# Kernel optimization log

Hardware: AMD Instinct MI355X
Metric: run time of the kernel (lower is better)

## Reference

```python
import jax, jax.numpy as jnp
import numpy as np

IN_DIM = 256
QK_DIM = IN_DIM // 8  # 32
NCLS = 19
B, H, W = 2, 64, 64


def conv3x3(x, w, b):
    # x: [B,C,H,W], w: [O,I,3,3] -> SAME padding, stride 1 (= pad=1 in torch)
    y = jax.lax.conv_general_dilated(x, w, (1, 1), 'SAME',
                                     dimension_numbers=('NCHW', 'OIHW', 'NCHW'))
    return y + b[None, :, None, None]


def setup_inputs() -> dict:
    key = jax.random.key(0)
    ks = jax.random.split(key, 20)
    s = 0.05
    inp = {
        'x': jax.random.normal(ks[0], (B, IN_DIM, H, W), jnp.float32),
        'modal_mask': jax.random.uniform(ks[1], (B, NCLS, H, W), jnp.float32),
        'amodal_mask': jax.random.uniform(ks[2], (B, NCLS, H, W), jnp.float32),
        'w_mp': jax.random.normal(ks[3], (NCLS, IN_DIM, 3, 3), jnp.float32) * s,
        'b_mp': jnp.zeros((NCLS,), jnp.float32),
        'w_ap': jax.random.normal(ks[4], (NCLS, IN_DIM, 3, 3), jnp.float32) * s,
        'b_ap': jnp.zeros((NCLS,), jnp.float32),
        'w_q': jax.random.normal(ks[5], (QK_DIM, IN_DIM + NCLS, 3, 3), jnp.float32) * s,
        'b_q': jnp.zeros((QK_DIM,), jnp.float32),
        'w_k': jax.random.normal(ks[6], (QK_DIM, IN_DIM + NCLS, 3, 3), jnp.float32) * s,
        'b_k': jnp.zeros((QK_DIM,), jnp.float32),
        'w_v': jax.random.normal(ks[7], (IN_DIM, IN_DIM, 3, 3), jnp.float32) * s,
        'b_v': jnp.zeros((IN_DIM,), jnp.float32),
        'w_comp': jax.random.normal(ks[8], (IN_DIM, IN_DIM + 2 * NCLS, 3, 3), jnp.float32) * s,
        'b_comp': jnp.zeros((IN_DIM,), jnp.float32),
        'w_out': jax.random.normal(ks[9], (IN_DIM, 3 * IN_DIM, 3, 3), jnp.float32) * s,
        'b_out': jnp.zeros((IN_DIM,), jnp.float32),
        # SELayer(in_dim, reduction=8): Linear(c, c//8, bias=False), Linear(c//8, c, bias=False)
        'w_se1': jax.random.normal(ks[10], (IN_DIM // 8, IN_DIM), jnp.float32) * s,
        'w_se2': jax.random.normal(ks[11], (IN_DIM, IN_DIM // 8), jnp.float32) * s,
    }
    return inp


def reference(x, modal_mask, amodal_mask, w_mp, b_mp, w_ap, b_ap, w_q, b_q,
              w_k, b_k, w_v, b_v, w_comp, b_comp, w_out, b_out, w_se1, w_se2):
    b, c, h, w = x.shape
    n = h * w
    # masks already at (h, w): nearest interpolate is identity
    modal_x = conv3x3(x, w_mp, b_mp) * modal_mask
    amodal_x = conv3x3(x, w_ap, b_ap) * amodal_mask
    inp = jnp.concatenate([x, modal_x, amodal_x], axis=1)
    out = conv3x3(inp, w_comp, b_comp)
    # SE layer
    y = out.mean(axis=(2, 3))                                # [b, c]
    y = jax.nn.sigmoid(jax.nn.relu(y @ w_se1.T) @ w_se2.T)   # [b, c]
    out_a = out * y[:, :, None, None]
    # dual-softmax spatial attention
    q = conv3x3(jnp.concatenate([x, modal_mask], axis=1), w_q, b_q).reshape(b, QK_DIM, n)
    k = conv3x3(jnp.concatenate([x, amodal_mask], axis=1), w_k, b_k).reshape(b, QK_DIM, n)
    v = conv3x3(x, w_v, b_v).reshape(b, c, n)
    energy = jnp.einsum('bdn,bdm->bnm', q, k)                # [b, n, n]
    attn = jax.nn.softmax(energy, axis=-1)                   # softmax over keys
    attn_t = jax.nn.softmax(energy, axis=1)                  # softmax over queries (of E^T rows)
    # out_b = bmm(v, attn^T); out_c = bmm(v, softmax(E^T,-1)^T)
    out_b = jnp.einsum('bcn,bmn->bcm', v, attn).reshape(b, c, h, w)
    out_c = jnp.einsum('bcn,bnm->bcm', v, attn_t).reshape(b, c, h, w)
    out = jnp.concatenate([out_a, out_b, out_c], axis=1)
    return conv3x3(out, w_out, b_out)
```

## Files before the change

kernel.cpp:

```cpp
#include <hip/hip_runtime.h>
#include <math.h>

#define HW 4096
#define IMG 64
#define PIX66 (66 * 66)

typedef short short8 __attribute__((ext_vector_type(8)));
typedef float f32x4 __attribute__((ext_vector_type(4)));

__device__ __forceinline__ unsigned short f2bf(float f) {
    unsigned int u = __float_as_uint(f);
    u += 0x7fff + ((u >> 16) & 1);
    return (unsigned short)(u >> 16);
}
__device__ __forceinline__ float bf2f(unsigned short h) {
    return __uint_as_float(((unsigned int)h) << 16);
}
__device__ __forceinline__ unsigned int pkbf(float a, float b) {
    unsigned int ua = __float_as_uint(a) + 0x8000u;
    unsigned int ub = __float_as_uint(b) + 0x8000u;
    return __builtin_amdgcn_perm(ub, ua, 0x07060302u);
}

__device__ __forceinline__ void gll16(const unsigned short* g, unsigned short* l) {
    __builtin_amdgcn_global_load_lds(
        (const __attribute__((address_space(1))) unsigned int*)(g),
        (__attribute__((address_space(3))) unsigned int*)(l), 16, 0, 0);
}

__device__ __forceinline__ int pxor(int pix) { return (pix ^ (pix >> 2)) & 3; }
__device__ __forceinline__ int p32o(int pix, int c) {
    return pix * 32 + ((((c >> 3) ^ pxor(pix)) & 3) << 3) + (c & 7);
}

struct WtJob {
    const float* w;
    unsigned short* dh;
    unsigned short* dl;
    int OC, OCpad, C0, K0pad, C1, Ktot;
};

__global__ __launch_bounds__(256) void k_wt_all(WtJob J0, WtJob J1, WtJob J2,
                                                WtJob J3, WtJob J4, WtJob J5,
                                                WtJob J6) {
    WtJob J;
    switch (blockIdx.y) {
        case 0: J = J0; break;
        case 1: J = J1; break;
        case 2: J = J2; break;
        case 3: J = J3; break;
        case 4: J = J4; break;
        case 5: J = J5; break;
        default: J = J6; break;
    }
    int idx = blockIdx.x * 256 + threadIdx.x;
    int KS = J.Ktot >> 5;
    int n = 9 * KS * J.OCpad * 32;
    if (idx >= n) return;
    int kk = idx & 31;
    int rest = idx >> 5;
    int oc = rest % J.OCpad;
    rest /= J.OCpad;
    int kg = rest % KS;
    int tap = rest / KS;
    int k = kg * 32 + kk;
    float v = 0.f;
    if (oc < J.OC) {
        int ic = -1;
        if (k < J.C0) ic = k;
        else if (k >= J.K0pad && (k - J.K0pad) < J.C1) ic = J.C0 + (k - J.K0pad);
        if (ic >= 0) v = J.w[((size_t)oc * (J.C0 + J.C1) + ic) * 9 + tap];
    }
    unsigned short hi = f2bf(v);
    J.dh[idx] = hi;
    if (J.dl) J.dl[idx] = f2bf(v - bf2f(hi));
}

__global__ __launch_bounds__(256) void k_build_x(const float* __restrict__ x,
                                                 unsigned short* __restrict__ xh,
                                                 unsigned short* __restrict__ xl,
                                                 unsigned short* __restrict__ ipad) {
    int b = blockIdx.z, c0 = blockIdx.y * 64, p0 = blockIdx.x * 64;
    __shared__ float s[64][65];
    int t = threadIdx.x;
    for (int i = t; i < 4096; i += 256) {
        int c = i >> 6, p = i & 63;
        s[p][c] = x[((size_t)b * 256 + c0 + c) * HW + p0 + p];
    }
    __syncthreads();
    for (int i = t; i < 4096; i += 256) {
        int c = i & 63, p = i >> 6;
        float f = s[p][c];
        unsigned short hi = f2bf(f);
        unsigned short lo = f2bf(f - bf2f(hi));
        int pp = p0 + p;
        int y = pp >> 6, xx = pp & 63;
        int pix = (y + 1) * 66 + xx + 1;
        int C = c0 + c;
        size_t ix = (size_t)(b * 8 + (C >> 5)) * (PIX66 * 32) + p32o(pix, C & 31);
        xh[ix] = hi;
        xl[ix] = lo;
        ipad[(size_t)(b * 10 + (C >> 5)) * (PIX66 * 32) + p32o(pix, C & 31)] = hi;
    }
}

__global__ __launch_bounds__(256) void k_build_mask2(
    const float* __restrict__ m0, const float* __restrict__ m1,
    unsigned short* __restrict__ d0h, unsigned short* __restrict__ d0l,
    unsigned short* __restrict__ d1h, unsigned short* __restrict__ d1l) {
    const float* m = blockIdx.y ? m1 : m0;
    unsigned short* dh = blockIdx.y ? d1h : d0h;
    unsigned short* dl = blockIdx.y ? d1l : d0l;
    int idx = blockIdx.x * 256 + threadIdx.x;
    int c = idx & 31;
    int p = (idx >> 5) & 4095;
    int b = idx >> 17;
    float f = (c < 19) ? m[((size_t)b * 19 + c) * HW + p] : 0.f;
    unsigned short hi = f2bf(f);
    int y = p >> 6, xx = p & 63;
    int pix = (y + 1) * 66 + xx + 1;
    dh[(size_t)b * (PIX66 * 32) + p32o(pix, c)] = hi;
    dl[(size_t)b * (PIX66 * 32) + p32o(pix, c)] = f2bf(f - bf2f(hi));
}

struct ConvJob {
    const unsigned short* s1h;
    const unsigned short* s1l;
    const unsigned short* wth;
    const unsigned short* wtl;
    const float* bias;
    unsigned short* d1;
    unsigned short* d2;
    const float* mask;
    int chBase;
};

template <int MODE, int SPLITK, int KS0, int KS1>
__global__ __launch_bounds__(256, 2) void conv_direct(
    const unsigned short* __restrict__ s0h, const unsigned short* __restrict__ s0l,
    ConvJob j0, ConvJob j1) {
    constexpr int KS = KS0 + KS1;
    constexpr int ST = 9 * KS;
    constexpr int DEPTH = SPLITK ? 2 : 4;
    int b = blockIdx.z;
    ConvJob J = blockIdx.y ? j1 : j0;
    int t = threadIdx.x, w = t >> 6, l = t & 63, quad = l >> 4, ln = l & 15;
    int pBase = blockIdx.x * 128 + w * 32;

    int padpix[2];
#pragma unroll
    for (int tn = 0; tn < 2; ++tn) {
        int p = pBase + tn * 16 + ln;
        padpix[tn] = ((p >> 6) + 1) * 66 + (p & 63) + 1;
    }
    size_t aoff[2];
#pragma unroll
    for (int tm = 0; tm < 2; ++tm) aoff[tm] = (size_t)(tm * 16 + ln) * 32 + quad * 8;

    const unsigned short* S0H = s0h + (size_t)b * KS0 * PIX66 * 32;
    const unsigned short* S0L = SPLITK ? s0l + (size_t)b * KS0 * PIX66 * 32
                                       : (const unsigned short*)0;
    const unsigned short* S1H = KS1 ? J.s1h + (size_t)b * KS1 * PIX66 * 32
                                    : (const unsigned short*)0;
    const unsigned short* S1L = (KS1 && SPLITK) ? J.s1l + (size_t)b * KS1 * PIX66 * 32
                                                : (const unsigned short*)0;

    f32x4 acc[2][2];
#pragma unroll
    for (int i = 0; i < 2; ++i)
#pragma unroll
        for (int j = 0; j < 2; ++j) acc[i][j] = (f32x4){0.f, 0.f, 0.f, 0.f};

    int tap = 0, kg = 0;
    auto adv = [&]() { if (++kg == KS) { kg = 0; ++tap; } };
    auto loadStep = [&](int ltap, int lkg, short8* bh, short8* bl, short8* ah,
                        short8* al) {
        int d3 = ltap / 3;
        int dpix = (d3 - 1) * 66 + (ltap - d3 * 3 - 1);
        const unsigned short* SpH;
        const unsigned short* SpL;
        long plane;
        if (lkg < KS0) {
            SpH = S0H; SpL = S0L; plane = (long)lkg * PIX66 * 32;
        } else {
            SpH = S1H; SpL = S1L; plane = (long)(lkg - KS0) * PIX66 * 32;
        }
#pragma unroll
        for (int tn = 0; tn < 2; ++tn) {
            int pix2 = padpix[tn] + dpix;
            long off = plane + (long)pix2 * 32 + (((quad ^ pxor(pix2)) & 3) << 3);
            bh[tn] = *(const short8*)(SpH + off);
            if (SPLITK) bl[tn] = *(const short8*)(SpL + off);
        }
        const unsigned short* WTh = J.wth + (size_t)(ltap * KS + lkg) * 32 * 32;
        ah[0] = *(const short8*)(WTh + aoff[0]);
        ah[1] = *(const short8*)(WTh + aoff[1]);
        if (SPLITK) {
            const unsigned short* WTl = J.wtl + (size_t)(ltap * KS + lkg) * 32 * 32;
            al[0] = *(const short8*)(WTl + aoff[0]);
            al[1] = *(const short8*)(WTl + aoff[1]);
        }
    };

    short8 BH[DEPTH][2], AH[DEPTH][2];
    short8 BL[SPLITK ? DEPTH : 1][2], AL[SPLITK ? DEPTH : 1][2];
#pragma unroll
    for (int u = 0; u < DEPTH; ++u) {
        loadStep(tap, kg, BH[u], BL[SPLITK ? u : 0], AH[u], AL[SPLITK ? u : 0]);
        adv();
    }

    for (int s = 0; s < ST; s += DEPTH) {
#pragma unroll
        for (int u = 0; u < DEPTH; ++u) {
            if (s + u < ST) {
#pragma unroll
                for (int tm = 0; tm < 2; ++tm)
#pragma unroll
                    for (int tn = 0; tn < 2; ++tn) {
                        acc[tm][tn] = __builtin_amdgcn_mfma_f32_16x16x32_bf16(
                            AH[u][tm], BH[u][tn], acc[tm][tn], 0, 0, 0);
                        if (SPLITK) {
                            acc[tm][tn] = __builtin_amdgcn_mfma_f32_16x16x32_bf16(
                                AL[u][tm], BH[u][tn], acc[tm][tn], 0, 0, 0);
                            acc[tm][tn] = __builtin_amdgcn_mfma_f32_16x16x32_bf16(
                                AH[u][tm], BL[u][tn], acc[tm][tn], 0, 0, 0);
                        }
                    }
                if (s + u + DEPTH < ST) {
                    loadStep(tap, kg, BH[u], BL[SPLITK ? u : 0], AH[u],
                             AL[SPLITK ? u : 0]);
                    adv();
                }
            }
        }
    }

#pragma unroll
    for (int tm = 0; tm < 2; ++tm) {
#pragma unroll
        for (int r = 0; r < 4; ++r) {
            int oc = tm * 16 + quad * 4 + r;
#pragma unroll
            for (int tn = 0; tn < 2; ++tn) {
                int p = pBase + tn * 16 + ln;
                if (MODE == 1) {
                    if (oc < 19) {
                        float v = (acc[tm][tn][r] + J.bias[oc]) *
                                  J.mask[((size_t)b * 19 + oc) * HW + p];
                        int ch = J.chBase + oc;
                        J.d1[(size_t)(b * 10 + (ch >> 5)) * (PIX66 * 32) +
                             p32o(padpix[tn], ch & 31)] = f2bf(v);
                    }
                } else {
                    float v = acc[tm][tn][r] + J.bias[oc];
                    unsigned short hi = f2bf(v);
                    J.d1[((size_t)b * HW + p) * 32 + oc] = hi;
                    J.d2[((size_t)b * HW + p) * 32 + oc] = f2bf(v - bf2f(hi));
                }
            }
        }
    }
}

struct LdsJob {
    const unsigned short* src;
    const unsigned short* wt;
    const float* bias;
    float* dstf;
    unsigned short* dstb;
    int KS;
    int mode;
};

__global__ __launch_bounds__(128, 3) void conv_lds(LdsJob j0, LdsJob j1,
                                                   int ocgPerJob,
                                                   float* __restrict__ ybuf) {
    int jy = blockIdx.y;
    LdsJob J = (jy >= ocgPerJob) ? j1 : j0;
    int ocBase = ((jy >= ocgPerJob) ? jy - ocgPerJob : jy) * 64;
    int z = blockIdx.z;
    int b = (J.mode == 5) ? (z & 1) : z;
    int kgBeg = 0, kgEnd = J.KS;
    if (J.mode == 5) {
        int half = J.KS >> 1;
        kgBeg = (z >> 1) * half;
        kgEnd = kgBeg + half;
    }
    int ry = blockIdx.x * 2;
    int t = threadIdx.x, w = t >> 6, l = t & 63, quad = l >> 4, ln = l & 15;

    __shared__ unsigned short sB[2][264 * 32];

    const unsigned short* S = J.src + (size_t)b * J.KS * PIX66 * 32;
    const size_t bStageBase = (size_t)(ry * 66) * 32;

    f32x4 acc[4][4];
#pragma unroll
    for (int i = 0; i < 4; ++i)
#pragma unroll
        for (int j = 0; j < 4; ++j) acc[i][j] = (f32x4){0.f, 0.f, 0.f, 0.f};

    {
        const unsigned short* gB = S + (size_t)kgBeg * PIX66 * 32 + bStageBase;
        for (int i = t; i < 1056; i += 128) gll16(gB + (size_t)i * 8, sB[0] + (size_t)i * 8);
    }

    for (int kg = kgBeg; kg < kgEnd; ++kg) {
        int cur = (kg - kgBeg) & 1;
        __syncthreads();
        if (kg + 1 < kgEnd) {
            const unsigned short* gB = S + (size_t)(kg + 1) * PIX66 * 32 + bStageBase;
            for (int i = t; i < 1056; i += 128)
                gll16(gB + (size_t)i * 8, sB[cur ^ 1] + (size_t)i * 8);
        }
        const unsigned short* sBc = sB[cur];
#pragma unroll
        for (int tap = 0; tap < 9; ++tap) {
            const unsigned short* gA =
                J.wt + ((size_t)(tap * J.KS + kg) * 256 + ocBase) * 32;
            int dy = tap / 3 - 1, dx = tap % 3 - 1;
            int lpBase = (1 + w + dy) * 66 + 1 + dx;
            short8 bf[4], af[4];
#pragma unroll
            for (int tn = 0; tn < 4; ++tn) {
                int lp = lpBase + tn * 16 + ln;
                int P = ry * 66 + lp;
                bf[tn] = *(const short8*)(sBc + (size_t)lp * 32 +
                                          (((quad ^ pxor(P)) & 3) << 3));
            }
#pragma unroll
            for (int tm = 0; tm < 4; ++tm)
                af[tm] = *(const short8*)(gA + (size_t)(tm * 16 + ln) * 32 + quad * 8);
#pragma unroll
            for (int tm = 0; tm < 4; ++tm)
#pragma unroll
                for (int tn = 0; tn < 4; ++tn)
                    acc[tm][tn] = __builtin_amdgcn_mfma_f32_16x16x32_bf16(
                        af[tm], bf[tn], acc[tm][tn], 0, 0, 0);
        }
    }

    int prow = ry + w;
#pragma unroll
    for (int tm = 0; tm < 4; ++tm) {
#pragma unroll
        for (int r = 0; r < 4; ++r) {
            int oc = ocBase + tm * 16 + quad * 4 + r;
            float msum = 0.f;
#pragma unroll
            for (int tn = 0; tn < 4; ++tn) {
                int px = tn * 16 + ln;
                if (J.mode == 5) {
                    J.dstf[((size_t)z * 256 + oc) * HW + prow * 64 + px] =
                        acc[tm][tn][r];
                } else if (J.mode == 3) {
                    int jc = ((px >> 3) ^ (oc & 7)) & 7;
                    J.dstb[(((size_t)b * 64 + prow) * 256 + oc) * 64 + jc * 8 +
                           (px & 7)] = f2bf(acc[tm][tn][r] + J.bias[oc]);
                } else {
                    float v = acc[tm][tn][r] + J.bias[oc];
                    int pix = (prow + 1) * 66 + px + 1;
                    J.dstb[(size_t)(b * 24 + (oc >> 5)) * (PIX66 * 32) +
                           p32o(pix, oc & 31)] = f2bf(v);
                    msum += v;
                }
            }
            if (J.mode == 4) {
#pragma unroll
                for (int off = 8; off; off >>= 1) msum += __shfl_down(msum, off, 16);
                if (ln == 0) atomicAdd(&ybuf[b * 256 + oc], msum);
            }
        }
    }
}

__global__ __launch_bounds__(256) void out_combine(const float* __restrict__ part,
                                                   const float* __restrict__ bias,
                                                   float* __restrict__ outp) {
    int idx = blockIdx.x * 256 + threadIdx.x;
    int p = idx & 4095;
    int oc = (idx >> 12) & 255;
    int b = idx >> 20;
    float v = part[((size_t)b * 256 + oc) * HW + p] +
              part[((size_t)(2 + b) * 256 + oc) * HW + p] + bias[oc];
    outp[((size_t)b * 256 + oc) * HW + p] = v;
}

__global__ __launch_bounds__(512, 4) void flash_attn(
    const unsigned short* __restrict__ qt_h, const unsigned short* __restrict__ qt_l,
    const unsigned short* __restrict__ kt_h, const unsigned short* __restrict__ kt_l,
    const unsigned short* __restrict__ vt,
    float* __restrict__ pO, float* __restrict__ pm, float* __restrict__ pl) {
    int seg = blockIdx.y >> 1, mode = blockIdx.y & 1, b = blockIdx.z;
    size_t qkoff = (size_t)b * HW * 32;
    const unsigned short* Qh = (mode ? kt_h : qt_h) + qkoff;
    const unsigned short* Ql = (mode ? kt_l : qt_l) + qkoff;
    const unsigned short* Kh = (mode ? qt_h : kt_h) + qkoff;
    const unsigned short* Kl = (mode ? qt_l : kt_l) + qkoff;
    const unsigned short* Vt = vt + (size_t)b * 64 * 256 * 64;

    int t = threadIdx.x, w = t >> 6, l = t & 63, quad = l >> 4, ln = l & 15;
    int pg = w & 1, ch = w >> 1;
    int p0 = blockIdx.x * 64, pw = pg * 32;
    int cb = ch * 64;
    bool soft = (ch == (pg ? 3 : 0));

    __shared__ unsigned short sV[256 * 64];
    __shared__ unsigned short sP[64 * 68];
    __shared__ float sAl[64];

    short8 qbh[2], qbl[2];
    if (soft) {
#pragma unroll
        for (int pn = 0; pn < 2; ++pn) {
            size_t off = (size_t)(p0 + pw + pn * 16 + ln) * 32 + quad * 8;
            qbh[pn] = *(const short8*)(Qh + off);
            qbl[pn] = *(const short8*)(Ql + off);
        }
    }

    float m_run[2] = {-3.0e38f, -3.0e38f};
    float l_run[2] = {0.f, 0.f};
    f32x4 accO[4][2];
#pragma unroll
    for (int cs = 0; cs < 4; ++cs)
#pragma unroll
        for (int pn = 0; pn < 2; ++pn) accO[cs][pn] = (f32x4){0.f, 0.f, 0.f, 0.f};

    int jbBeg = seg * (HW / 2);
    for (int jb = jbBeg; jb < jbBeg + HW / 2; jb += 64) {
        __syncthreads();
        {
            const unsigned short* gV = Vt + (size_t)(jb >> 6) * (256 * 64);
#pragma unroll
            for (int i = 0; i < 4; ++i)
                gll16(gV + (size_t)(t + 512 * i) * 8, sV + (size_t)(t + 512 * i) * 8);
        }
        if (soft) {
            f32x4 sacc[2][4];
#pragma unroll
            for (int pn = 0; pn < 2; ++pn)
#pragma unroll
                for (int jj = 0; jj < 4; ++jj) sacc[pn][jj] = (f32x4){0.f, 0.f, 0.f, 0.f};
#pragma unroll
            for (int jj = 0; jj < 4; ++jj) {
                size_t off = (size_t)(jb + 16 * jj + ln) * 32 + quad * 8;
                short8 kh = *(const short8*)(Kh + off);
                short8 kr = *(const short8*)(Kl + off);
#pragma unroll
                for (int pn = 0; pn < 2; ++pn) {
                    sacc[pn][jj] = __builtin_amdgcn_mfma_f32_16x16x32_bf16(
                        kh, qbh[pn], sacc[pn][jj], 0, 0, 0);
                    sacc[pn][jj] = __builtin_amdgcn_mfma_f32_16x16x32_bf16(
                        kh, qbl[pn], sacc[pn][jj], 0, 0, 0);
                    sacc[pn][jj] = __builtin_amdgcn_mfma_f32_16x16x32_bf16(
                        kr, qbh[pn], sacc[pn][jj], 0, 0, 0);
                }
            }
#pragma unroll
            for (int pn = 0; pn < 2; ++pn) {
                float tmx = -3.0e38f;
#pragma unroll
                for (int jj = 0; jj < 4; ++jj)
#pragma unroll
                    for (int r = 0; r < 4; ++r) tmx = fmaxf(tmx, sacc[pn][jj][r]);
                tmx = fmaxf(tmx, __shfl_xor(tmx, 16));
                tmx = fmaxf(tmx, __shfl_xor(tmx, 32));
                float mnew = fmaxf(m_run[pn], tmx);
                float alpha = __expf(m_run[pn] - mnew);
                m_run[pn] = mnew;
                float psum = 0.f;
#pragma unroll
                for (int jj = 0; jj < 4; ++jj) {
                    float e0 = __expf(sacc[pn][jj][0] - mnew);
                    float e1 = __expf(sacc[pn][jj][1] - mnew);
                    float e2 = __expf(sacc[pn][jj][2] - mnew);
                    float e3 = __expf(sacc[pn][jj][3] - mnew);
                    psum += (e0 + e1) + (e2 + e3);
                    uint2 pk;
                    pk.x = pkbf(e0, e1);
                    pk.y = pkbf(e2, e3);
                    *(uint2*)(sP + (size_t)(pw + pn * 16 + ln) * 68 + jj * 16 +
                              quad * 4) = pk;
                }
                psum += __shfl_xor(psum, 16);
                psum += __shfl_xor(psum, 32);
                l_run[pn] = l_run[pn] * alpha + psum;
                if (quad == 0) sAl[pw + pn * 16 + ln] = alpha;
            }
        }
        __syncthreads();
        float al0 = sAl[pw + ln];
        float al1 = sAl[pw + 16 + ln];
#pragma unroll
        for (int cs = 0; cs < 4; ++cs) { accO[cs][0] *= al0; accO[cs][1] *= al1; }
#pragma unroll
        for (int j2 = 0; j2 < 2; ++j2) {
            short8 pb0 = *(const short8*)(sP + (size_t)(pw + ln) * 68 + j2 * 32 +
                                          quad * 8);
            short8 pb1 = *(const short8*)(sP + (size_t)(pw + 16 + ln) * 68 + j2 * 32 +
                                          quad * 8);
#pragma unroll
            for (int cs = 0; cs < 4; ++cs) {
                int c = cb + cs * 16 + ln;
                short8 va = *(const short8*)(
                    sV + (size_t)c * 64 + ((((j2 * 4 + quad) ^ (c & 7)) & 7) << 3));
                accO[cs][0] = __builtin_amdgcn_mfma_f32_16x16x32_bf16(
                    va, pb0, accO[cs][0], 0, 0, 0);
                accO[cs][1] = __builtin_amdgcn_mfma_f32_16x16x32_bf16(
                    va, pb1, accO[cs][1], 0, 0, 0);
            }
        }
    }

    int idx4 = (seg * 2 + mode) * 2 + b;
#pragma unroll
    for (int pn = 0; pn < 2; ++pn) {
        int p = p0 + pw + pn * 16 + ln;
        if (soft && quad == 0) {
            pm[(size_t)idx4 * HW + p] = m_run[pn];
            pl[(size_t)idx4 * HW + p] = l_run[pn];
        }
#pragma unroll
        for (int cs = 0; cs < 4; ++cs)
#pragma unroll
            for (int r = 0; r < 4; ++r) {
                int c = cb + cs * 16 + quad * 4 + r;
                pO[((size_t)idx4 * 256 + c) * HW + p] = accO[cs][pn][r];
            }
    }
}

__global__ __launch_bounds__(256) void attn_combine(const float* __restrict__ pO,
                                                    const float* __restrict__ pm,
                                                    const float* __restrict__ pl,
                                                    unsigned short* __restrict__ catN) {
    int b = blockIdx.z, mode = blockIdx.y;
    int t = threadIdx.x;
    int p = blockIdx.x * 64 + (t & 63);
    int c0 = (t >> 6) * 64;
    int i0 = mode * 2 + b;
    int i1 = 4 + mode * 2 + b;
    float m0 = pm[(size_t)i0 * HW + p], m1 = pm[(size_t)i1 * HW + p];
    float l0 = pl[(size_t)i0 * HW + p], l1 = pl[(size_t)i1 * HW + p];
    float M = fmaxf(m0, m1);
    float e0 = __expf(m0 - M), e1 = __expf(m1 - M);
    float inv = 1.f / (l0 * e0 + l1 * e1);
    e0 *= inv;
    e1 *= inv;
    int y = p >> 6, x = p & 63;
    int pix = (y + 1) * 66 + x + 1;
    for (int c = c0; c < c0 + 64; ++c) {
        float v = pO[((size_t)i0 * 256 + c) * HW + p] * e0 +
                  pO[((size_t)i1 * 256 + c) * HW + p] * e1;
        int cf = 256 + mode * 256 + c;
        catN[(size_t)(b * 24 + (cf >> 5)) * (PIX66 * 32) + p32o(pix, cf & 31)] = f2bf(v);
    }
}

__global__ __launch_bounds__(256) void se_mlp_kernel(const float* __restrict__ y,
                                                     const float* __restrict__ w1,
                                                     const float* __restrict__ w2,
                                                     float* __restrict__ sc) {
    int b = blockIdx.x, t = threadIdx.x;
    __shared__ float sy[256], sh[32];
    sy[t] = y[b * 256 + t] * (1.f / 4096.f);
    __syncthreads();
    if (t < 32) {
        float s = 0.f;
        for (int c = 0; c < 256; ++c) s = fmaf(w1[t * 256 + c], sy[c], s);
        sh[t] = fmaxf(s, 0.f);
    }
    __syncthreads();
    float s = 0.f;
#pragma unroll
    for (int h = 0; h < 32; ++h) s = fmaf(w2[t * 32 + h], sh[h], s);
    sc[b * 256 + t] = 1.f / (1.f + __expf(-s));
}

__global__ __launch_bounds__(256) void se_scale_cat(unsigned short* __restrict__ catN,
                                                    const float* __restrict__ sc) {
    int idx = blockIdx.x * 256 + threadIdx.x;
    int c = idx & 255;
    int p = (idx >> 8) & 4095;
    int b = idx >> 20;
    int y = p >> 6, x = p & 63;
    int pix = (y + 1) * 66 + x + 1;
    unsigned short* q =
        catN + (size_t)(b * 24 + (c >> 5)) * (PIX66 * 32) + p32o(pix, c & 31);
    *q = f2bf(bf2f(*q) * sc[b * 256 + c]);
}

extern "C" void kernel_launch(void* const* d_in, const int* in_sizes, int n_in,
                              void* d_out, int out_size, void* d_ws, size_t ws_size,
                              hipStream_t stream) {
    const float* x      = (const float*)d_in[0];
    const float* mmask  = (const float*)d_in[1];
    const float* amask  = (const float*)d_in[2];
    const float* w_mp   = (const float*)d_in[3];
    const float* b_mp   = (const float*)d_in[4];
    const float* w_ap   = (const float*)d_in[5];
    const float* b_ap   = (const float*)d_in[6];
    const float* w_q    = (const float*)d_in[7];
    const float* b_q    = (const float*)d_in[8];
    const float* w_k    = (const float*)d_in[9];
    const float* b_k    = (const float*)d_in[10];
    const float* w_v    = (const float*)d_in[11];
    const float* b_v    = (const float*)d_in[12];
    const float* w_comp = (const float*)d_in[13];
    const float* b_comp = (const float*)d_in[14];
    const float* w_out  = (const float*)d_in[15];
    const float* b_out  = (const float*)d_in[16];
    const float* w_se1  = (const float*)d_in[17];
    const float* w_se2  = (const float*)d_in[18];

    unsigned short* us = (unsigned short*)d_ws;
    size_t o = 0;
    unsigned short* xpad_hi = us + o; o += (size_t)2 * 8 * PIX66 * 32;
    unsigned short* xpad_lo = us + o; o += (size_t)2 * 8 * PIX66 * 32;
    unsigned short* mq_hi   = us + o; o += (size_t)2 * PIX66 * 32;
    unsigned short* mq_lo   = us + o; o += (size_t)2 * PIX66 * 32;
    unsigned short* ma_hi   = us + o; o += (size_t)2 * PIX66 * 32;
    unsigned short* ma_lo   = us + o; o += (size_t)2 * PIX66 * 32;
    unsigned short* ipad    = us + o; o += (size_t)2 * 10 * PIX66 * 32;
    unsigned short* catN    = us + o; o += (size_t)2 * 24 * PIX66 * 32;
    size_t zeroBytes = o * sizeof(unsigned short);
    unsigned short* wt_mp = us + o; o += (size_t)9 * 8 * 32 * 32;
    unsigned short* wt_ap = us + o; o += (size_t)9 * 8 * 32 * 32;
    unsigned short* wt_qh = us + o; o += (size_t)9 * 9 * 32 * 32;
    unsigned short* wt_ql = us + o; o += (size_t)9 * 9 * 32 * 32;
    unsigned short* wt_kh = us + o; o += (size_t)9 * 9 * 32 * 32;
    unsigned short* wt_kl = us + o; o += (size_t)9 * 9 * 32 * 32;
    unsigned short* wt_v  = us + o; o += (size_t)9 * 8 * 256 * 32;
    unsigned short* wt_cp = us + o; o += (size_t)9 * 10 * 256 * 32;
    unsigned short* wt_ot = us + o; o += (size_t)9 * 24 * 256 * 32;
    unsigned short* qt_h  = us + o; o += (size_t)2 * HW * 32;
    unsigned short* qt_l  = us + o; o += (size_t)2 * HW * 32;
    unsigned short* kt_h  = us + o; o += (size_t)2 * HW * 32;
    unsigned short* kt_l  = us + o; o += (size_t)2 * HW * 32;
    unsigned short* vt    = us + o; o += (size_t)2 * 64 * 256 * 64;
    float* fp = (float*)(us + o);
    size_t fo = 0;
    float* pAtt = fp + fo; fo += (size_t)8 * 256 * HW;
    float* pmb  = fp + fo; fo += (size_t)8 * HW;
    float* plb  = fp + fo; fo += (size_t)8 * HW;
    float* pOut = fp + fo; fo += (size_t)4 * 256 * HW;
    float* ybuf = fp + fo; fo += 512;
    float* sbuf = fp + fo; fo += 512;
    size_t need = o * sizeof(unsigned short) + fo * sizeof(float);
    if (ws_size < need) return;

    float* outp = (float*)d_out;

    hipMemsetAsync(us, 0, zeroBytes, stream);
    hipMemsetAsync(ybuf, 0, 512 * sizeof(float), stream);

    WtJob W0{w_mp,   wt_mp, (unsigned short*)0, 19, 32, 256, 256, 0, 256};
    WtJob W1{w_ap,   wt_ap, (unsigned short*)0, 19, 32, 256, 256, 0, 256};
    WtJob W2{w_q,    wt_qh, wt_ql,             32, 32, 256, 256, 19, 288};
    WtJob W3{w_k,    wt_kh, wt_kl,             32, 32, 256, 256, 19, 288};
    WtJob W4{w_v,    wt_v,  (unsigned short*)0, 256, 256, 256, 256, 0, 256};
    WtJob W5{w_comp, wt_cp, (unsigned short*)0, 256, 256, 294, 320, 0, 320};
    WtJob W6{w_out,  wt_ot, (unsigned short*)0, 256, 256, 768, 768, 0, 768};
    k_wt_all<<<dim3((9 * 24 * 256 * 32 + 255) / 256, 7), 256, 0, stream>>>(
        W0, W1, W2, W3, W4, W5, W6);

    k_build_x<<<dim3(64, 4, 2), 256, 0, stream>>>(x, xpad_hi, xpad_lo, ipad);
    k_build_mask2<<<dim3(1024, 2), 256, 0, stream>>>(mmask, amask, mq_hi, mq_lo,
                                                     ma_hi, ma_lo);

    const unsigned short* NUS = (const unsigned short*)0;
    unsigned short* NUSo = (unsigned short*)0;
    float* NF = (float*)0;

    ConvJob jm{NUS, NUS, wt_mp, NUS, b_mp, ipad, NUSo, mmask, 256};
    ConvJob ja{NUS, NUS, wt_ap, NUS, b_ap, ipad, NUSo, amask, 275};
    conv_direct<1, 0, 8, 0><<<dim3(32, 2, 2), 256, 0, stream>>>(xpad_hi, NUS, jm, ja);

    ConvJob jq{mq_hi, mq_lo, wt_qh, wt_ql, b_q, qt_h, qt_l, NF, 0};
    ConvJob jk{ma_hi, ma_lo, wt_kh, wt_kl, b_k, kt_h, kt_l, NF, 0};
    conv_direct<2, 1, 8, 1><<<dim3(32, 2, 2), 256, 0, stream>>>(xpad_hi, xpad_lo, jq, jk);

    LdsJob jv{xpad_hi, wt_v, b_v, NF, vt, 8, 3};
    LdsJob jc{ipad, wt_cp, b_comp, NF, catN, 10, 4};
    conv_lds<<<dim3(32, 8, 2), 128, 0, stream>>>(jv, jc, 4, ybuf);

    se_mlp_kernel<<<2, 256, 0, stream>>>(ybuf, w_se1, w_se2, sbuf);
    se_scale_cat<<<8192, 256, 0, stream>>>(catN, sbuf);

    flash_attn<<<dim3(64, 4, 2), 512, 0, stream>>>(qt_h, qt_l, kt_h, kt_l, vt,
                                                   pAtt, pmb, plb);
    attn_combine<<<dim3(64, 2, 2), 256, 0, stream>>>(pAtt, pmb, plb, catN);

    LdsJob jo{catN, wt_ot, NF, pOut, NUSo, 24, 5};
    conv_lds<<<dim3(32, 4, 4), 128, 0, stream>>>(jo, jo, 4, NF);
    out_combine<<<8192, 256, 0, stream>>>(pOut, b_out, outp);
}
```

Measured before the change: 498.1 us.

## Pipeline softmax ahead of PV in flash attention and shrink conv_direct blocks

The flash attention kernel double-buffers the probability tile and alpha arrays so the two softmax warps compute QK and softmax for the next key block while the other warps run the PV MFMAs for the current one. Channel work is rebalanced: softmax warps now handle only 16 channels and the other six warps 80 each, instead of every warp taking 64. Separately, conv_direct drops to 128-thread blocks with twice as many blocks to improve occupancy and load spread. This costs extra LDS for the double buffers, more accumulator registers in the non-softmax warps, and an extra sync per iteration.

```diff
diff --git a/kernel.cpp b/kernel.cpp
--- a/kernel.cpp
+++ b/kernel.cpp
@@ -136,7 +136,7 @@
 };
 
 template <int MODE, int SPLITK, int KS0, int KS1>
-__global__ __launch_bounds__(256, 2) void conv_direct(
+__global__ __launch_bounds__(128, 2) void conv_direct(
     const unsigned short* __restrict__ s0h, const unsigned short* __restrict__ s0l,
     ConvJob j0, ConvJob j1) {
     constexpr int KS = KS0 + KS1;
@@ -145,7 +145,7 @@
     int b = blockIdx.z;
     ConvJob J = blockIdx.y ? j1 : j0;
     int t = threadIdx.x, w = t >> 6, l = t & 63, quad = l >> 4, ln = l & 15;
-    int pBase = blockIdx.x * 128 + w * 32;
+    int pBase = blockIdx.x * 64 + w * 32;
 
     int padpix[2];
 #pragma unroll
@@ -401,14 +401,15 @@
     const unsigned short* Vt = vt + (size_t)b * 64 * 256 * 64;
 
     int t = threadIdx.x, w = t >> 6, l = t & 63, quad = l >> 4, ln = l & 15;
-    int pg = w & 1, ch = w >> 1;
+    int pg = w & 1, sl = w >> 1;
+    bool soft = (sl == (pg ? 3 : 0));
     int p0 = blockIdx.x * 64, pw = pg * 32;
-    int cb = ch * 64;
-    bool soft = (ch == (pg ? 3 : 0));
+    int cbS = pg ? 240 : 0;
+    int cbP = pg ? (sl * 80) : (16 + (sl - 1) * 80);
 
     __shared__ unsigned short sV[256 * 64];
-    __shared__ unsigned short sP[64 * 68];
-    __shared__ float sAl[64];
+    __shared__ unsigned short sP[2][64 * 68];
+    __shared__ float sAl[2][64];
 
     short8 qbh[2], qbl[2];
     if (soft) {
@@ -422,113 +423,157 @@
 
     float m_run[2] = {-3.0e38f, -3.0e38f};
     float l_run[2] = {0.f, 0.f};
-    f32x4 accO[4][2];
-#pragma unroll
-    for (int cs = 0; cs < 4; ++cs)
-#pragma unroll
-        for (int pn = 0; pn < 2; ++pn) accO[cs][pn] = (f32x4){0.f, 0.f, 0.f, 0.f};
+    f32x4 accS[2];
+    f32x4 accP[5][2];
+    accS[0] = (f32x4){0.f, 0.f, 0.f, 0.f};
+    accS[1] = (f32x4){0.f, 0.f, 0.f, 0.f};
+#pragma unroll
+    for (int cs = 0; cs < 5; ++cs) {
+        accP[cs][0] = (f32x4){0.f, 0.f, 0.f, 0.f};
+        accP[cs][1] = (f32x4){0.f, 0.f, 0.f, 0.f};
+    }
 
     int jbBeg = seg * (HW / 2);
-    for (int jb = jbBeg; jb < jbBeg + HW / 2; jb += 64) {
+    const int NT = (HW / 2) / 64;
+
+    auto qkstep = [&](int it2) {
+        int jb = jbBeg + it2 * 64;
+        int nb = it2 & 1;
+        f32x4 sacc[2][4];
+#pragma unroll
+        for (int pn = 0; pn < 2; ++pn)
+#pragma unroll
+            for (int jj = 0; jj < 4; ++jj) sacc[pn][jj] = (f32x4){0.f, 0.f, 0.f, 0.f};
+#pragma unroll
+        for (int jj = 0; jj < 4; ++jj) {
+            size_t off = (size_t)(jb + 16 * jj + ln) * 32 + quad * 8;
+            short8 kh = *(const short8*)(Kh + off);
+            short8 kr = *(const short8*)(Kl + off);
+#pragma unroll
+            for (int pn = 0; pn < 2; ++pn) {
+                sacc[pn][jj] = __builtin_amdgcn_mfma_f32_16x16x32_bf16(
+                    kh, qbh[pn], sacc[pn][jj], 0, 0, 0);
+                sacc[pn][jj] = __builtin_amdgcn_mfma_f32_16x16x32_bf16(
+                    kh, qbl[pn], sacc[pn][jj], 0, 0, 0);
+                sacc[pn][jj] = __builtin_amdgcn_mfma_f32_16x16x32_bf16(
+                    kr, qbh[pn], sacc[pn][jj], 0, 0, 0);
+            }
+        }
+#pragma unroll
+        for (int pn = 0; pn < 2; ++pn) {
+            float tmx = -3.0e38f;
+#pragma unroll
+            for (int jj = 0; jj < 4; ++jj)
+#pragma unroll
+                for (int r = 0; r < 4; ++r) tmx = fmaxf(tmx, sacc[pn][jj][r]);
+            tmx = fmaxf(tmx, __shfl_xor(tmx, 16));
+            tmx = fmaxf(tmx, __shfl_xor(tmx, 32));
+            float mnew = fmaxf(m_run[pn], tmx);
+            float alpha = __expf(m_run[pn] - mnew);
+            m_run[pn] = mnew;
+            float psum = 0.f;
+#pragma unroll
+            for (int jj = 0; jj < 4; ++jj) {
+                float e0 = __expf(sacc[pn][jj][0] - mnew);
+                float e1 = __expf(sacc[pn][jj][1] - mnew);
+                float e2 = __expf(sacc[pn][jj][2] - mnew);
+                float e3 = __expf(sacc[pn][jj][3] - mnew);
+                psum += (e0 + e1) + (e2 + e3);
+                uint2 pk;
+                pk.x = pkbf(e0, e1);
+                pk.y = pkbf(e2, e3);
+                *(uint2*)(sP[nb] + (size_t)(pw + pn * 16 + ln) * 68 + jj * 16 +
+                          quad * 4) = pk;
+            }
+            psum += __shfl_xor(psum, 16);
+            psum += __shfl_xor(psum, 32);
+            l_run[pn] = l_run[pn] * alpha + psum;
+            if (quad == 0) sAl[nb][pw + pn * 16 + ln] = alpha;
+        }
+    };
+
+    if (soft) qkstep(0);
+
+    for (int it = 0; it < NT; ++it) {
+        int cur = it & 1;
         __syncthreads();
         {
-            const unsigned short* gV = Vt + (size_t)(jb >> 6) * (256 * 64);
+            const unsigned short* gV = Vt + (size_t)((jbBeg >> 6) + it) * (256 * 64);
 #pragma unroll
             for (int i = 0; i < 4; ++i)
                 gll16(gV + (size_t)(t + 512 * i) * 8, sV + (size_t)(t + 512 * i) * 8);
         }
+        if (soft && it + 1 < NT) qkstep(it + 1);
+        __syncthreads();
         if (soft) {
-            f32x4 sacc[2][4];
-#pragma unroll
-            for (int pn = 0; pn < 2; ++pn)
-#pragma unroll
-                for (int jj = 0; jj < 4; ++jj) sacc[pn][jj] = (f32x4){0.f, 0.f, 0.f, 0.f};
-#pragma unroll
-            for (int jj = 0; jj < 4; ++jj) {
-                size_t off = (size_t)(jb + 16 * jj + ln) * 32 + quad * 8;
-                short8 kh = *(const short8*)(Kh + off);
-                short8 kr = *(const short8*)(Kl + off);
-#pragma unroll
-                for (int pn = 0; pn < 2; ++pn) {
-                    sacc[pn][jj] = __builtin_amdgcn_mfma_f32_16x16x32_bf16(
-                        kh, qbh[pn], sacc[pn][jj], 0, 0, 0);
-                    sacc[pn][jj] = __builtin_amdgcn_mfma_f32_16x16x32_bf16(
-                        kh, qbl[pn], sacc[pn][jj], 0, 0, 0);
-                    sacc[pn][jj] = __builtin_amdgcn_mfma_f32_16x16x32_bf16(
-                        kr, qbh[pn], sacc[pn][jj], 0, 0, 0);
-                }
-            }
-#pragma unroll
-            for (int pn = 0; pn < 2; ++pn) {
-                float tmx = -3.0e38f;
-#pragma unroll
-                for (int jj = 0; jj < 4; ++jj)
-#pragma unroll
-                    for (int r = 0; r < 4; ++r) tmx = fmaxf(tmx, sacc[pn][jj][r]);
-                tmx = fmaxf(tmx, __shfl_xor(tmx, 16));
-                tmx = fmaxf(tmx, __shfl_xor(tmx, 32));
-                float mnew = fmaxf(m_run[pn], tmx);
-                float alpha = __expf(m_run[pn] - mnew);
-                m_run[pn] = mnew;
-                float psum = 0.f;
-#pragma unroll
-                for (int jj = 0; jj < 4; ++jj) {
-                    float e0 = __expf(sacc[pn][jj][0] - mnew);
-                    float e1 = __expf(sacc[pn][jj][1] - mnew);
-                    float e2 = __expf(sacc[pn][jj][2] - mnew);
-                    float e3 = __expf(sacc[pn][jj][3] - mnew);
-                    psum += (e0 + e1) + (e2 + e3);
-                    uint2 pk;
-                    pk.x = pkbf(e0, e1);
-                    pk.y = pkbf(e2, e3);
-                    *(uint2*)(sP + (size_t)(pw + pn * 16 + ln) * 68 + jj * 16 +
-                              quad * 4) = pk;
-                }
-                psum += __shfl_xor(psum, 16);
-                psum += __shfl_xor(psum, 32);
-                l_run[pn] = l_run[pn] * alpha + psum;
-                if (quad == 0) sAl[pw + pn * 16 + ln] = alpha;
-            }
-        }
-        __syncthreads();
-        float al0 = sAl[pw + ln];
-        float al1 = sAl[pw + 16 + ln];
-#pragma unroll
-        for (int cs = 0; cs < 4; ++cs) { accO[cs][0] *= al0; accO[cs][1] *= al1; }
-#pragma unroll
-        for (int j2 = 0; j2 < 2; ++j2) {
-            short8 pb0 = *(const short8*)(sP + (size_t)(pw + ln) * 68 + j2 * 32 +
-                                          quad * 8);
-            short8 pb1 = *(const short8*)(sP + (size_t)(pw + 16 + ln) * 68 + j2 * 32 +
-                                          quad * 8);
-#pragma unroll
-            for (int cs = 0; cs < 4; ++cs) {
-                int c = cb + cs * 16 + ln;
+            float a0 = sAl[cur][pw + ln], a1 = sAl[cur][pw + 16 + ln];
+            accS[0] *= a0;
+            accS[1] *= a1;
+#pragma unroll
+            for (int j2 = 0; j2 < 2; ++j2) {
+                short8 pb0 = *(const short8*)(sP[cur] + (size_t)(pw + ln) * 68 +
+                                              j2 * 32 + quad * 8);
+                short8 pb1 = *(const short8*)(sP[cur] + (size_t)(pw + 16 + ln) * 68 +
+                                              j2 * 32 + quad * 8);
+                int c = cbS + ln;
                 short8 va = *(const short8*)(
                     sV + (size_t)c * 64 + ((((j2 * 4 + quad) ^ (c & 7)) & 7) << 3));
-                accO[cs][0] = __builtin_amdgcn_mfma_f32_16x16x32_bf16(
-                    va, pb0, accO[cs][0], 0, 0, 0);
-                accO[cs][1] = __builtin_amdgcn_mfma_f32_16x16x32_bf16(
-                    va, pb1, accO[cs][1], 0, 0, 0);
+                accS[0] = __builtin_amdgcn_mfma_f32_16x16x32_bf16(va, pb0, accS[0],
+                                                                  0, 0, 0);
+                accS[1] = __builtin_amdgcn_mfma_f32_16x16x32_bf16(va, pb1, accS[1],
+                                                                  0, 0, 0);
+            }
+        } else {
+            float a0 = sAl[cur][pw + ln], a1 = sAl[cur][pw + 16 + ln];
+#pragma unroll
+            for (int cs = 0; cs < 5; ++cs) { accP[cs][0] *= a0; accP[cs][1] *= a1; }
+#pragma unroll
+            for (int j2 = 0; j2 < 2; ++j2) {
+                short8 pb0 = *(const short8*)(sP[cur] + (size_t)(pw + ln) * 68 +
+                                              j2 * 32 + quad * 8);
+                short8 pb1 = *(const short8*)(sP[cur] + (size_t)(pw + 16 + ln) * 68 +
+                                              j2 * 32 + quad * 8);
+#pragma unroll
+                for (int cs = 0; cs < 5; ++cs) {
+                    int c = cbP + cs * 16 + ln;
+                    short8 va = *(const short8*)(
+                        sV + (size_t)c * 64 + ((((j2 * 4 + quad) ^ (c & 7)) & 7) << 3));
+                    accP[cs][0] = __builtin_amdgcn_mfma_f32_16x16x32_bf16(
+                        va, pb0, accP[cs][0], 0, 0, 0);
+                    accP[cs][1] = __builtin_amdgcn_mfma_f32_16x16x32_bf16(
+                        va, pb1, accP[cs][1], 0, 0, 0);
+                }
             }
         }
     }
 
     int idx4 = (seg * 2 + mode) * 2 + b;
-#pragma unroll
-    for (int pn = 0; pn < 2; ++pn) {
-        int p = p0 + pw + pn * 16 + ln;
-        if (soft && quad == 0) {
-            pm[(size_t)idx4 * HW + p] = m_run[pn];
-            pl[(size_t)idx4 * HW + p] = l_run[pn];
-        }
-#pragma unroll
-        for (int cs = 0; cs < 4; ++cs)
+    if (soft) {
+#pragma unroll
+        for (int pn = 0; pn < 2; ++pn) {
+            int p = p0 + pw + pn * 16 + ln;
+            if (quad == 0) {
+                pm[(size_t)idx4 * HW + p] = m_run[pn];
+                pl[(size_t)idx4 * HW + p] = l_run[pn];
+            }
 #pragma unroll
             for (int r = 0; r < 4; ++r) {
-                int c = cb + cs * 16 + quad * 4 + r;
-                pO[((size_t)idx4 * 256 + c) * HW + p] = accO[cs][pn][r];
-            }
+                int c = cbS + quad * 4 + r;
+                pO[((size_t)idx4 * 256 + c) * HW + p] = accS[pn][r];
+            }
+        }
+    } else {
+#pragma unroll
+        for (int pn = 0; pn < 2; ++pn) {
+            int p = p0 + pw + pn * 16 + ln;
+#pragma unroll
+            for (int cs = 0; cs < 5; ++cs)
+#pragma unroll
+                for (int r = 0; r < 4; ++r) {
+                    int c = cbP + cs * 16 + quad * 4 + r;
+                    pO[((size_t)idx4 * 256 + c) * HW + p] = accP[cs][pn][r];
+                }
+        }
     }
 }
 
@@ -676,11 +721,11 @@
 
     ConvJob jm{NUS, NUS, wt_mp, NUS, b_mp, ipad, NUSo, mmask, 256};
     ConvJob ja{NUS, NUS, wt_ap, NUS, b_ap, ipad, NUSo, amask, 275};
-    conv_direct<1, 0, 8, 0><<<dim3(32, 2, 2), 256, 0, stream>>>(xpad_hi, NUS, jm, ja);
+    conv_direct<1, 0, 8, 0><<<dim3(64, 2, 2), 128, 0, stream>>>(xpad_hi, NUS, jm, ja);
 
     ConvJob jq{mq_hi, mq_lo, wt_qh, wt_ql, b_q, qt_h, qt_l, NF, 0};
     ConvJob jk{ma_hi, ma_lo, wt_kh, wt_kl, b_k, kt_h, kt_l, NF, 0};
-    conv_direct<2, 1, 8, 1><<<dim3(32, 2, 2), 256, 0, stream>>>(xpad_hi, xpad_lo, jq, jk);
+    conv_direct<2, 1, 8, 1><<<dim3(64, 2, 2), 128, 0, stream>>>(xpad_hi, xpad_lo, jq, jk);
 
     LdsJob jv{xpad_hi, wt_v, b_v, NF, vt, 8, 3};
     LdsJob jc{ipad, wt_cp, b_comp, NF, catN, 10, 4};
```

Result: slower. 520.2 us (+4.4%).

## Merge direct convs into one launch and split-K the LDS convs for more blocks

Applied to the files above, without the earlier changes.

Replaces the two templated direct-conv launches with a single runtime-dispatched kernel covering the modal, amodal, q and k jobs, using 128-thread blocks and twice as many blocks. The v and comp LDS convs are split over two K segments and the output conv over four, writing fp32 partials. New combine kernels add the bias, apply the SE scale and convert to bf16, and the separate SE rescale pass is dropped. The aim is better CU occupancy on a small problem, paid for with extra partial-sum memory traffic, more launches, and runtime branches in place of compile-time specialisation.

```diff
diff --git a/kernel.cpp b/kernel.cpp
--- a/kernel.cpp
+++ b/kernel.cpp
@@ -123,7 +123,7 @@
     dl[(size_t)b * (PIX66 * 32) + p32o(pix, c)] = f2bf(f - bf2f(hi));
 }
 
-struct ConvJob {
+struct DJob {
     const unsigned short* s1h;
     const unsigned short* s1l;
     const unsigned short* wth;
@@ -133,19 +133,27 @@
     unsigned short* d2;
     const float* mask;
     int chBase;
+    int mode;
+    int split;
+    int KS1;
 };
 
-template <int MODE, int SPLITK, int KS0, int KS1>
-__global__ __launch_bounds__(256, 2) void conv_direct(
+__global__ __launch_bounds__(128, 2) void conv_direct_all(
     const unsigned short* __restrict__ s0h, const unsigned short* __restrict__ s0l,
-    ConvJob j0, ConvJob j1) {
-    constexpr int KS = KS0 + KS1;
-    constexpr int ST = 9 * KS;
-    constexpr int DEPTH = SPLITK ? 2 : 4;
+    DJob j0, DJob j1, DJob j2, DJob j3) {
+    DJob J;
+    switch (blockIdx.y) {
+        case 0: J = j0; break;
+        case 1: J = j1; break;
+        case 2: J = j2; break;
+        default: J = j3; break;
+    }
+    const int KS0 = 8;
+    int KS = KS0 + J.KS1;
+    int ST = 9 * KS;
     int b = blockIdx.z;
-    ConvJob J = blockIdx.y ? j1 : j0;
     int t = threadIdx.x, w = t >> 6, l = t & 63, quad = l >> 4, ln = l & 15;
-    int pBase = blockIdx.x * 128 + w * 32;
+    int pBase = blockIdx.x * 64 + w * 32;
 
     int padpix[2];
 #pragma unroll
@@ -158,12 +166,11 @@
     for (int tm = 0; tm < 2; ++tm) aoff[tm] = (size_t)(tm * 16 + ln) * 32 + quad * 8;
 
     const unsigned short* S0H = s0h + (size_t)b * KS0 * PIX66 * 32;
-    const unsigned short* S0L = SPLITK ? s0l + (size_t)b * KS0 * PIX66 * 32
-                                       : (const unsigned short*)0;
-    const unsigned short* S1H = KS1 ? J.s1h + (size_t)b * KS1 * PIX66 * 32
-                                    : (const unsigned short*)0;
-    const unsigned short* S1L = (KS1 && SPLITK) ? J.s1l + (size_t)b * KS1 * PIX66 * 32
-                                                : (const unsigned short*)0;
+    const unsigned short* S0L = s0l + (size_t)b * KS0 * PIX66 * 32;
+    const unsigned short* S1H = J.KS1 ? J.s1h + (size_t)b * PIX66 * 32
+                                      : (const unsigned short*)0;
+    const unsigned short* S1L = J.KS1 ? J.s1l + (size_t)b * PIX66 * 32
+                                      : (const unsigned short*)0;
 
     f32x4 acc[2][2];
 #pragma unroll
@@ -183,36 +190,32 @@
         if (lkg < KS0) {
             SpH = S0H; SpL = S0L; plane = (long)lkg * PIX66 * 32;
         } else {
-            SpH = S1H; SpL = S1L; plane = (long)(lkg - KS0) * PIX66 * 32;
+            SpH = S1H; SpL = S1L; plane = 0;
         }
 #pragma unroll
         for (int tn = 0; tn < 2; ++tn) {
             int pix2 = padpix[tn] + dpix;
             long off = plane + (long)pix2 * 32 + (((quad ^ pxor(pix2)) & 3) << 3);
             bh[tn] = *(const short8*)(SpH + off);
-            if (SPLITK) bl[tn] = *(const short8*)(SpL + off);
+            if (J.split) bl[tn] = *(const short8*)(SpL + off);
         }
         const unsigned short* WTh = J.wth + (size_t)(ltap * KS + lkg) * 32 * 32;
         ah[0] = *(const short8*)(WTh + aoff[0]);
         ah[1] = *(const short8*)(WTh + aoff[1]);
-        if (SPLITK) {
+        if (J.split) {
             const unsigned short* WTl = J.wtl + (size_t)(ltap * KS + lkg) * 32 * 32;
             al[0] = *(const short8*)(WTl + aoff[0]);
             al[1] = *(const short8*)(WTl + aoff[1]);
         }
     };
 
-    short8 BH[DEPTH][2], AH[DEPTH][2];
-    short8 BL[SPLITK ? DEPTH : 1][2], AL[SPLITK ? DEPTH : 1][2];
-#pragma unroll
-    for (int u = 0; u < DEPTH; ++u) {
-        loadStep(tap, kg, BH[u], BL[SPLITK ? u : 0], AH[u], AL[SPLITK ? u : 0]);
-        adv();
-    }
-
-    for (int s = 0; s < ST; s += DEPTH) {
-#pragma unroll
-        for (int u = 0; u < DEPTH; ++u) {
+    short8 BH[2][2], AH[2][2], BL[2][2], AL[2][2];
+#pragma unroll
+    for (int u = 0; u < 2; ++u) { loadStep(tap, kg, BH[u], BL[u], AH[u], AL[u]); adv(); }
+
+    for (int s = 0; s < ST; s += 2) {
+#pragma unroll
+        for (int u = 0; u < 2; ++u) {
             if (s + u < ST) {
 #pragma unroll
                 for (int tm = 0; tm < 2; ++tm)
@@ -220,18 +223,14 @@
                     for (int tn = 0; tn < 2; ++tn) {
                         acc[tm][tn] = __builtin_amdgcn_mfma_f32_16x16x32_bf16(
                             AH[u][tm], BH[u][tn], acc[tm][tn], 0, 0, 0);
-                        if (SPLITK) {
+                        if (J.split) {
                             acc[tm][tn] = __builtin_amdgcn_mfma_f32_16x16x32_bf16(
                                 AL[u][tm], BH[u][tn], acc[tm][tn], 0, 0, 0);
                             acc[tm][tn] = __builtin_amdgcn_mfma_f32_16x16x32_bf16(
                                 AH[u][tm], BL[u][tn], acc[tm][tn], 0, 0, 0);
                         }
                     }
-                if (s + u + DEPTH < ST) {
-                    loadStep(tap, kg, BH[u], BL[SPLITK ? u : 0], AH[u],
-                             AL[SPLITK ? u : 0]);
-                    adv();
-                }
+                if (s + u + 2 < ST) { loadStep(tap, kg, BH[u], BL[u], AH[u], AL[u]); adv(); }
             }
         }
     }
@@ -244,7 +243,7 @@
 #pragma unroll
             for (int tn = 0; tn < 2; ++tn) {
                 int p = pBase + tn * 16 + ln;
-                if (MODE == 1) {
+                if (J.mode == 1) {
                     if (oc < 19) {
                         float v = (acc[tm][tn][r] + J.bias[oc]) *
                                   J.mask[((size_t)b * 19 + oc) * HW + p];
@@ -263,30 +262,24 @@
     }
 }
 
-struct LdsJob {
+struct LJob {
     const unsigned short* src;
     const unsigned short* wt;
-    const float* bias;
     float* dstf;
-    unsigned short* dstb;
     int KS;
-    int mode;
+    int nseg;
+    int doSum;
 };
 
-__global__ __launch_bounds__(128, 3) void conv_lds(LdsJob j0, LdsJob j1,
-                                                   int ocgPerJob,
+__global__ __launch_bounds__(128, 3) void conv_lds(LJob j0, LJob j1, int ocgPerJob,
                                                    float* __restrict__ ybuf) {
     int jy = blockIdx.y;
-    LdsJob J = (jy >= ocgPerJob) ? j1 : j0;
+    LJob J = (jy >= ocgPerJob) ? j1 : j0;
     int ocBase = ((jy >= ocgPerJob) ? jy - ocgPerJob : jy) * 64;
     int z = blockIdx.z;
-    int b = (J.mode == 5) ? (z & 1) : z;
-    int kgBeg = 0, kgEnd = J.KS;
-    if (J.mode == 5) {
-        int half = J.KS >> 1;
-        kgBeg = (z >> 1) * half;
-        kgEnd = kgBeg + half;
-    }
+    int b = z & 1, seg = z >> 1;
+    int kgPer = J.KS / J.nseg;
+    int kgBeg = seg * kgPer, kgEnd = kgBeg + kgPer;
     int ry = blockIdx.x * 2;
     int t = threadIdx.x, w = t >> 6, l = t & 63, quad = l >> 4, ln = l & 15;
 
@@ -351,28 +344,46 @@
 #pragma unroll
             for (int tn = 0; tn < 4; ++tn) {
                 int px = tn * 16 + ln;
-                if (J.mode == 5) {
-                    J.dstf[((size_t)z * 256 + oc) * HW + prow * 64 + px] =
-                        acc[tm][tn][r];
-                } else if (J.mode == 3) {
-                    int jc = ((px >> 3) ^ (oc & 7)) & 7;
-                    J.dstb[(((size_t)b * 64 + prow) * 256 + oc) * 64 + jc * 8 +
-                           (px & 7)] = f2bf(acc[tm][tn][r] + J.bias[oc]);
-                } else {
-                    float v = acc[tm][tn][r] + J.bias[oc];
-                    int pix = (prow + 1) * 66 + px + 1;
-                    J.dstb[(size_t)(b * 24 + (oc >> 5)) * (PIX66 * 32) +
-                           p32o(pix, oc & 31)] = f2bf(v);
-                    msum += v;
-                }
-            }
-            if (J.mode == 4) {
+                J.dstf[((size_t)z * 256 + oc) * HW + prow * 64 + px] = acc[tm][tn][r];
+                msum += acc[tm][tn][r];
+            }
+            if (J.doSum) {
 #pragma unroll
                 for (int off = 8; off; off >>= 1) msum += __shfl_down(msum, off, 16);
                 if (ln == 0) atomicAdd(&ybuf[b * 256 + oc], msum);
             }
         }
     }
+}
+
+__global__ __launch_bounds__(256) void vt_combine(const float* __restrict__ part,
+                                                  const float* __restrict__ bias,
+                                                  unsigned short* __restrict__ vt) {
+    int idx = blockIdx.x * 256 + threadIdx.x;
+    int p = idx & 4095;
+    int oc = (idx >> 12) & 255;
+    int b = idx >> 20;
+    float v = part[((size_t)b * 256 + oc) * HW + p] +
+              part[((size_t)(2 + b) * 256 + oc) * HW + p] + bias[oc];
+    int prow = p >> 6, px = p & 63;
+    int jc = ((px >> 3) ^ (oc & 7)) & 7;
+    vt[(((size_t)b * 64 + prow) * 256 + oc) * 64 + jc * 8 + (px & 7)] = f2bf(v);
+}
+
+__global__ __launch_bounds__(256) void comp_combine(const float* __restrict__ part,
+                                                    const float* __restrict__ bias,
+                                                    const float* __restrict__ sc,
+                                                    unsigned short* __restrict__ catN) {
+    int idx = blockIdx.x * 256 + threadIdx.x;
+    int p = idx & 4095;
+    int oc = (idx >> 12) & 255;
+    int b = idx >> 20;
+    float v = (part[((size_t)b * 256 + oc) * HW + p] +
+               part[((size_t)(2 + b) * 256 + oc) * HW + p] + bias[oc]) *
+              sc[b * 256 + oc];
+    int prow = p >> 6, px = p & 63;
+    int pix = (prow + 1) * 66 + px + 1;
+    catN[(size_t)(b * 24 + (oc >> 5)) * (PIX66 * 32) + p32o(pix, oc & 31)] = f2bf(v);
 }
 
 __global__ __launch_bounds__(256) void out_combine(const float* __restrict__ part,
@@ -382,8 +393,10 @@
     int p = idx & 4095;
     int oc = (idx >> 12) & 255;
     int b = idx >> 20;
-    float v = part[((size_t)b * 256 + oc) * HW + p] +
-              part[((size_t)(2 + b) * 256 + oc) * HW + p] + bias[oc];
+    float v = part[((size_t)(0 + b) * 256 + oc) * HW + p] +
+              part[((size_t)(2 + b) * 256 + oc) * HW + p] +
+              part[((size_t)(4 + b) * 256 + oc) * HW + p] +
+              part[((size_t)(6 + b) * 256 + oc) * HW + p] + bias[oc];
     outp[((size_t)b * 256 + oc) * HW + p] = v;
 }
 
@@ -560,12 +573,13 @@
 }
 
 __global__ __launch_bounds__(256) void se_mlp_kernel(const float* __restrict__ y,
+                                                     const float* __restrict__ bcomp,
                                                      const float* __restrict__ w1,
                                                      const float* __restrict__ w2,
                                                      float* __restrict__ sc) {
     int b = blockIdx.x, t = threadIdx.x;
     __shared__ float sy[256], sh[32];
-    sy[t] = y[b * 256 + t] * (1.f / 4096.f);
+    sy[t] = y[b * 256 + t] * (1.f / 4096.f) + bcomp[t];
     __syncthreads();
     if (t < 32) {
         float s = 0.f;
@@ -577,19 +591,6 @@
 #pragma unroll
     for (int h = 0; h < 32; ++h) s = fmaf(w2[t * 32 + h], sh[h], s);
     sc[b * 256 + t] = 1.f / (1.f + __expf(-s));
-}
-
-__global__ __launch_bounds__(256) void se_scale_cat(unsigned short* __restrict__ catN,
-                                                    const float* __restrict__ sc) {
-    int idx = blockIdx.x * 256 + threadIdx.x;
-    int c = idx & 255;
-    int p = (idx >> 8) & 4095;
-    int b = idx >> 20;
-    int y = p >> 6, x = p & 63;
-    int pix = (y + 1) * 66 + x + 1;
-    unsigned short* q =
-        catN + (size_t)(b * 24 + (c >> 5)) * (PIX66 * 32) + p32o(pix, c & 31);
-    *q = f2bf(bf2f(*q) * sc[b * 256 + c]);
 }
 
 extern "C" void kernel_launch(void* const* d_in, const int* in_sizes, int n_in,
@@ -645,7 +646,9 @@
     float* pAtt = fp + fo; fo += (size_t)8 * 256 * HW;
     float* pmb  = fp + fo; fo += (size_t)8 * HW;
     float* plb  = fp + fo; fo += (size_t)8 * HW;
-    float* pOut = fp + fo; fo += (size_t)4 * 256 * HW;
+    float* pOut = fp + fo; fo += (size_t)8 * 256 * HW;
+    float* pV   = fp + fo; fo += (size_t)4 * 256 * HW;
+    float* pC   = fp + fo; fo += (size_t)4 * 256 * HW;
     float* ybuf = fp + fo; fo += 512;
     float* sbuf = fp + fo; fo += 512;
     size_t need = o * sizeof(unsigned short) + fo * sizeof(float);
@@ -674,26 +677,25 @@
     unsigned short* NUSo = (unsigned short*)0;
     float* NF = (float*)0;
 
-    ConvJob jm{NUS, NUS, wt_mp, NUS, b_mp, ipad, NUSo, mmask, 256};
-    ConvJob ja{NUS, NUS, wt_ap, NUS, b_ap, ipad, NUSo, amask, 275};
-    conv_direct<1, 0, 8, 0><<<dim3(32, 2, 2), 256, 0, stream>>>(xpad_hi, NUS, jm, ja);
-
-    ConvJob jq{mq_hi, mq_lo, wt_qh, wt_ql, b_q, qt_h, qt_l, NF, 0};
-    ConvJob jk{ma_hi, ma_lo, wt_kh, wt_kl, b_k, kt_h, kt_l, NF, 0};
-    conv_direct<2, 1, 8, 1><<<dim3(32, 2, 2), 256, 0, stream>>>(xpad_hi, xpad_lo, jq, jk);
-
-    LdsJob jv{xpad_hi, wt_v, b_v, NF, vt, 8, 3};
-    LdsJob jc{ipad, wt_cp, b_comp, NF, catN, 10, 4};
-    conv_lds<<<dim3(32, 8, 2), 128, 0, stream>>>(jv, jc, 4, ybuf);
-
-    se_mlp_kernel<<<2, 256, 0, stream>>>(ybuf, w_se1, w_se2, sbuf);
-    se_scale_cat<<<8192, 256, 0, stream>>>(catN, sbuf);
+    DJob dm{NUS, NUS, wt_mp, NUS, b_mp, ipad, NUSo, mmask, 256, 1, 0, 0};
+    DJob da{NUS, NUS, wt_ap, NUS, b_ap, ipad, NUSo, amask, 275, 1, 0, 0};
+    DJob dq{mq_hi, mq_lo, wt_qh, wt_ql, b_q, qt_h, qt_l, NF, 0, 2, 1, 1};
+    DJob dk{ma_hi, ma_lo, wt_kh, wt_kl, b_k, kt_h, kt_l, NF, 0, 2, 1, 1};
+    conv_direct_all<<<dim3(64, 4, 2), 128, 0, stream>>>(xpad_hi, xpad_lo, dm, da, dq, dk);
+
+    LJob lv{xpad_hi, wt_v, pV, 8, 2, 0};
+    LJob lc{ipad, wt_cp, pC, 10, 2, 1};
+    conv_lds<<<dim3(32, 8, 4), 128, 0, stream>>>(lv, lc, 4, ybuf);
+
+    se_mlp_kernel<<<2, 256, 0, stream>>>(ybuf, b_comp, w_se1, w_se2, sbuf);
+    vt_combine<<<8192, 256, 0, stream>>>(pV, b_v, vt);
+    comp_combine<<<8192, 256, 0, stream>>>(pC, b_comp, sbuf, catN);
 
     flash_attn<<<dim3(64, 4, 2), 512, 0, stream>>>(qt_h, qt_l, kt_h, kt_l, vt,
                                                    pAtt, pmb, plb);
     attn_combine<<<dim3(64, 2, 2), 256, 0, stream>>>(pAtt, pmb, plb, catN);
 
-    LdsJob jo{catN, wt_ot, NF, pOut, NUSo, 24, 5};
-    conv_lds<<<dim3(32, 4, 4), 128, 0, stream>>>(jo, jo, 4, NF);
+    LJob lo{catN, wt_ot, pOut, 24, 4, 0};
+    conv_lds<<<dim3(32, 4, 8), 128, 0, stream>>>(lo, lo, 4, NF);
     out_combine<<<8192, 256, 0, stream>>>(pOut, b_out, outp);
 }
```

Measured after the change: 424.2 us. -14.8%, faster.
